# Optimization experiments

Hardware: AMD Instinct MI355X
Metric: run time of the kernel (lower is better)

## Reference

```python
import jax, jax.numpy as jnp
import numpy as np

BN_EPS = 1e-5


def _conv2d(x, w, pad):
    # x: [B,C,H,W], w: [O,I,kh,kw]
    return jax.lax.conv_general_dilated(
        x, w, window_strides=(1, 1), padding=((pad, pad), (pad, pad)),
        dimension_numbers=("NCHW", "OIHW", "NCHW"))


def _feat(x, conv_w, bn_gamma, bn_beta, bn_mean, bn_var, desc_w, desc_b):
    # BasicConv(64->32, k=3, pad=1): conv (no bias) -> BN (inference) -> ReLU
    y = _conv2d(x, conv_w, pad=1)
    inv = bn_gamma / jnp.sqrt(bn_var + BN_EPS)
    y = y * inv[None, :, None, None] + (bn_beta - bn_mean * inv)[None, :, None, None]
    y = jnp.maximum(y, 0.0)
    # desc: 1x1 conv 32->32 with bias
    y = _conv2d(y, desc_w, pad=0) + desc_b[None, :, None, None]
    return y  # [B,32,H,W]


def setup_inputs() -> dict:
    key = jax.random.key(0)
    ks = jax.random.split(key, 4)
    B, Cin, H, W = 8, 64, 160, 576
    left = jax.random.normal(ks[0], (B, Cin, H, W), dtype=jnp.float32)
    right = jax.random.normal(ks[1], (B, Cin, H, W), dtype=jnp.float32)
    conv_w = jax.random.normal(ks[2], (32, 64, 3, 3), dtype=jnp.float32) * 0.05
    bn_gamma = jnp.ones((32,), jnp.float32)
    bn_beta = jnp.zeros((32,), jnp.float32)
    bn_mean = jnp.zeros((32,), jnp.float32)
    bn_var = jnp.ones((32,), jnp.float32)
    desc_w = jax.random.normal(ks[3], (32, 32, 1, 1), dtype=jnp.float32) * 0.1
    desc_b = jnp.zeros((32,), jnp.float32)
    return {"left": left, "right": right, "conv_w": conv_w,
            "bn_gamma": bn_gamma, "bn_beta": bn_beta,
            "bn_mean": bn_mean, "bn_var": bn_var,
            "desc_w": desc_w, "desc_b": desc_b, "maxdisp": 48}


def reference(left, right, conv_w, bn_gamma, bn_beta, bn_mean, bn_var,
              desc_w, desc_b, maxdisp):
    L = _feat(left, conv_w, bn_gamma, bn_beta, bn_mean, bn_var, desc_w, desc_b)
    R = _feat(right, conv_w, bn_gamma, bn_beta, bn_mean, bn_var, desc_w, desc_b)
    # reduce_mean is a frozen 1x1 conv with weight 1/32 == mean over channels.
    cv = [jnp.mean(L * R, axis=1)]  # d = 0, [B,H,W]
    for d in range(1, maxdisp):  # maxdisp is a static Python int (structural)
        c = jnp.mean(L[:, :, :, d:] * R[:, :, :, :-d], axis=1)  # [B,H,W-d]
        cv.append(jnp.pad(c, ((0, 0), (0, 0), (d, 0))))  # zero-pad left edge
    return jnp.stack(cv, axis=1)  # [B, maxdisp, H, W]
```

## Files before the change

### kernel.cpp

```cpp
#include <hip/hip_runtime.h>
#include <stdint.h>

#define HH   160
#define WW   576
#define CIN  64
#define BATCH 8
#define MAXD 48

typedef unsigned int  uint;
typedef unsigned short ushort;
typedef __attribute__((ext_vector_type(8))) short bf16x8;
typedef __attribute__((ext_vector_type(4))) float f32x4;
typedef __attribute__((ext_vector_type(16))) float f32x16;

static constexpr size_t WTB_OFF  = 0;
static constexpr size_t DWT_OFF  = 36864;
static constexpr size_t B1_OFF   = 38912;
static constexpr size_t B2_OFF   = 39040;
static constexpr size_t FEAT_OFF = 40960;
static constexpr size_t FEAT_ELEMS = (size_t)BATCH * HH * WW * 32;

__device__ __forceinline__ uint f2bf(float f) {
    uint u = __float_as_uint(f);
    u = (u + 0x7fffu + ((u >> 16) & 1u)) >> 16;
    return u;
}
__device__ __forceinline__ float bf2f_lo(uint u) { return __uint_as_float(u << 16); }
__device__ __forceinline__ float bf2f_hi(uint u) { return __uint_as_float(u & 0xffff0000u); }
__device__ __forceinline__ uint pk2(float a, float b) { return f2bf(a) | (f2bf(b) << 16); }

__global__ void prep_kernel(const float* __restrict__ conv_w,
                            const float* __restrict__ gamma,
                            const float* __restrict__ beta,
                            const float* __restrict__ mean,
                            const float* __restrict__ var,
                            const float* __restrict__ desc_w,
                            const float* __restrict__ desc_b,
                            char* __restrict__ ws) {
    int tid = blockIdx.x * 256 + threadIdx.x;
    ushort* wtB = (ushort*)(ws + WTB_OFF);
    ushort* dwt = (ushort*)(ws + DWT_OFF);
    float*  b1  = (float*)(ws + B1_OFF);
    float*  b2  = (float*)(ws + B2_OFF);
    if (tid < 36 * 64 * 8) {
        int j    = tid & 7;
        int l    = (tid >> 3) & 63;
        int f    = tid >> 9;
        int s    = f & 3;
        int tap  = f >> 2;
        int ch = l & 31;
        int ci = s * 16 + (l >> 5) * 8 + j;
        float inv = gamma[ch] * rsqrtf(var[ch] + 1e-5f);
        wtB[tid] = (ushort)f2bf(conv_w[(size_t)(ch * 64 + ci) * 9 + tap] * inv);
    }
    if (tid < 1024) {
        int j = tid & 7;
        int l = (tid >> 3) & 63;
        int s = tid >> 9;
        int o = l & 31;
        int mid = (j & 3) + 8 * (j >> 2) + 16 * s + 4 * (l >> 5);
        dwt[tid] = (ushort)f2bf(desc_w[o * 32 + mid]);
    }
    if (tid < 32) {
        float inv = gamma[tid] * rsqrtf(var[tid] + 1e-5f);
        b1[tid] = beta[tid] - mean[tid] * inv;
        b2[tid] = desc_b[tid];
    }
}

#define NXB 6
#define NYB 40
#define NWG (NXB * NYB * 2 * BATCH)
__global__ __launch_bounds__(256, 4)
void feat_mfma(const float* __restrict__ left,
               const float* __restrict__ right,
               const char* __restrict__ ws,
               ushort* __restrict__ featL,
               ushort* __restrict__ featR) {
    __shared__ __align__(16) ushort tile[2 * 600 * 8];

    int bid = blockIdx.x;
    int nid = (bid & 7) * (NWG / 8) + (bid >> 3);
    int x    = nid % NXB;
    int rest = nid / NXB;
    int hy   = rest % NYB;
    int z    = rest / NYB;
    int b    = z & 7;
    const float* __restrict__ in = (z < 8 ? left : right) + (size_t)b * CIN * HH * WW;
    ushort* __restrict__ feat = (z < 8 ? featL : featR);
    const int w0 = x * 96;
    const int h0 = hy * 4;
    const int PL = HH * WW;

    const int lane = threadIdx.x & 63;
    const int wv   = threadIdx.x >> 6;
    const int n    = lane & 31;
    const int hi   = lane >> 5;

    const ushort* __restrict__ wtB = (const ushort*)(ws + WTB_OFF);

    f32x16 acc[3] = {};

    for (int chunk = 0; chunk < 4; ++chunk) {
        for (int t = threadIdx.x; t < 1536; t += 256) {
            int lpx  = t & 63;
            int seg  = t >> 6;
            int part = seg & 1;
            int oct  = (seg >> 1) & 1;
            int r    = seg >> 2;
            int px   = part * 64 + lpx;
            if (px < 100) {
                int gh = h0 + r - 1;
                int gw = w0 - 1 + px;
                float f0 = 0.f, f1 = 0.f, f2 = 0.f, f3 = 0.f,
                      f4 = 0.f, f5 = 0.f, f6 = 0.f, f7 = 0.f;
                if (((unsigned)gh < HH) && ((unsigned)gw < WW)) {
                    const float* src = in + (size_t)(chunk * 16 + oct * 8) * PL
                                          + (size_t)gh * WW + gw;
                    f0 = src[0];
                    f1 = src[(size_t)PL];
                    f2 = src[(size_t)2 * PL];
                    f3 = src[(size_t)3 * PL];
                    f4 = src[(size_t)4 * PL];
                    f5 = src[(size_t)5 * PL];
                    f6 = src[(size_t)6 * PL];
                    f7 = src[(size_t)7 * PL];
                }
                uint4 o4;
                o4.x = pk2(f0, f1);
                o4.y = pk2(f2, f3);
                o4.z = pk2(f4, f5);
                o4.w = pk2(f6, f7);
                *(uint4*)&tile[(size_t)(oct * 600 + r * 100 + px) * 8] = o4;
            }
        }
        __syncthreads();

#pragma unroll
        for (int tap = 0; tap < 9; ++tap) {
            const int r = tap / 3, kw = tap % 3;
            bf16x8 a = *(const bf16x8*)(wtB + (size_t)((tap * 4 + chunk) * 64 + lane) * 8);
#pragma unroll
            for (int tl = 0; tl < 3; ++tl) {
                int px = (wv + r) * 100 + tl * 32 + n + kw;
                bf16x8 bb = *(const bf16x8*)&tile[(size_t)(hi * 600 + px) * 8];
                acc[tl] = __builtin_amdgcn_mfma_f32_32x32x16_bf16(a, bb, acc[tl], 0, 0, 0);
            }
        }
        __syncthreads();
    }

    const float* __restrict__ b1 = (const float*)(ws + B1_OFF);
    const float* __restrict__ b2 = (const float*)(ws + B2_OFF);
    f32x4 b1q[4], b2q[4];
#pragma unroll
    for (int q = 0; q < 4; ++q) {
        b1q[q] = *(const f32x4*)(b1 + 8 * q + 4 * hi);
        b2q[q] = *(const f32x4*)(b2 + 8 * q + 4 * hi);
    }
    const ushort* __restrict__ dwt = (const ushort*)(ws + DWT_OFF);
    bf16x8 da0 = *(const bf16x8*)(dwt + (size_t)lane * 8);
    bf16x8 da1 = *(const bf16x8*)(dwt + (size_t)(64 + lane) * 8);

#pragma unroll
    for (int tl = 0; tl < 3; ++tl) {
        bf16x8 p0, p1;
#pragma unroll
        for (int j = 0; j < 8; ++j) {
            float v0 = fmaxf(acc[tl][j]     + b1q[j >> 2][j & 3],       0.f);
            float v1 = fmaxf(acc[tl][8 + j] + b1q[2 + (j >> 2)][j & 3], 0.f);
            p0[j] = (short)f2bf(v0);
            p1[j] = (short)f2bf(v1);
        }
        f32x16 acc2;
#pragma unroll
        for (int j = 0; j < 16; ++j) acc2[j] = b2q[j >> 2][j & 3];
        acc2 = __builtin_amdgcn_mfma_f32_32x32x16_bf16(da0, p0, acc2, 0, 0, 0);
        acc2 = __builtin_amdgcn_mfma_f32_32x32x16_bf16(da1, p1, acc2, 0, 0, 0);

        size_t pix = ((size_t)b * HH + h0 + wv) * WW + w0 + tl * 32 + n;
        ushort* fp = feat + pix * 32 + 4 * hi;
#pragma unroll
        for (int q = 0; q < 4; ++q) {
            uint u0 = pk2(acc2[4 * q],     acc2[4 * q + 1]);
            uint u1 = pk2(acc2[4 * q + 2], acc2[4 * q + 3]);
            *(uint2*)(fp + 8 * q) = make_uint2(u0, u1);
        }
    }
}

#define CVT 192
__global__ __launch_bounds__(CVT)
void cv_kernel(const ushort* __restrict__ featL,
               const ushort* __restrict__ featR,
               float* __restrict__ out) {
    __shared__ ushort r_lds[WW * 40];

    const int t  = threadIdx.x;
    const int bh = blockIdx.x;
    const int b  = bh / HH;
    const int h  = bh - b * HH;
    const ushort* __restrict__ Lrow = featL + ((size_t)b * HH + h) * WW * 32;
    const ushort* __restrict__ Rrow = featR + ((size_t)b * HH + h) * WW * 32;

#pragma unroll
    for (int k = 0; k < 3; ++k) {
        int w = t + k * CVT;
        const uint4* src = (const uint4*)(Rrow + (size_t)w * 32);
        uint4* dst = (uint4*)(r_lds + (size_t)w * 40);
#pragma unroll
        for (int j = 0; j < 4; ++j) dst[j] = src[j];
    }

    float Lf[3][32];
#pragma unroll
    for (int k = 0; k < 3; ++k) {
        int w = t + k * CVT;
        const uint4* src = (const uint4*)(Lrow + (size_t)w * 32);
#pragma unroll
        for (int j = 0; j < 4; ++j) {
            uint4 v = src[j];
            uint vv[4] = {v.x, v.y, v.z, v.w};
#pragma unroll
            for (int q = 0; q < 4; ++q) {
                Lf[k][j * 8 + q * 2]     = bf2f_lo(vv[q]);
                Lf[k][j * 8 + q * 2 + 1] = bf2f_hi(vv[q]);
            }
        }
    }
    __syncthreads();

    float* __restrict__ outBase = out + ((size_t)b * MAXD * HH + h) * WW;
    for (int d = 0; d < MAXD; ++d) {
#pragma unroll
        for (int k = 0; k < 3; ++k) {
            int w = t + k * CVT;
            float res = 0.f;
            if (w >= d) {
                const uint4* rp = (const uint4*)(r_lds + (size_t)(w - d) * 40);
                float s0 = 0.f, s1 = 0.f;
#pragma unroll
                for (int j = 0; j < 4; ++j) {
                    uint4 v = rp[j];
                    uint vv[4] = {v.x, v.y, v.z, v.w};
#pragma unroll
                    for (int q = 0; q < 4; ++q) {
                        int idx = j * 8 + q * 2;
                        s0 = fmaf(Lf[k][idx],     bf2f_lo(vv[q]), s0);
                        s1 = fmaf(Lf[k][idx + 1], bf2f_hi(vv[q]), s1);
                    }
                }
                res = (s0 + s1) * (1.f / 32.f);
            }
            outBase[(size_t)d * HH * WW + w] = res;
        }
    }
}

extern "C" void kernel_launch(void* const* d_in, const int* in_sizes, int n_in,
                              void* d_out, int out_size, void* d_ws, size_t ws_size,
                              hipStream_t stream) {
    const float* left   = (const float*)d_in[0];
    const float* right  = (const float*)d_in[1];
    const float* conv_w = (const float*)d_in[2];
    const float* gamma  = (const float*)d_in[3];
    const float* beta   = (const float*)d_in[4];
    const float* mean   = (const float*)d_in[5];
    const float* var    = (const float*)d_in[6];
    const float* desc_w = (const float*)d_in[7];
    const float* desc_b = (const float*)d_in[8];
    float*  out   = (float*)d_out;
    char*   ws    = (char*)d_ws;
    ushort* featL = (ushort*)(ws + FEAT_OFF);
    ushort* featR = featL + FEAT_ELEMS;

    prep_kernel<<<72, 256, 0, stream>>>(conv_w, gamma, beta, mean, var, desc_w, desc_b, ws);
    feat_mfma<<<NWG, 256, 0, stream>>>(left, right, ws, featL, featR);
    cv_kernel<<<BATCH * HH, CVT, 0, stream>>>(featL, featR, out);
}
```

Baseline: 252.2 us.

## Double-buffer LDS input tile and overlap global loads with MFMA taps

```diff
diff --git a/kernel.cpp b/kernel.cpp
--- a/kernel.cpp
+++ b/kernel.cpp
@@ -77,7 +77,7 @@
                const char* __restrict__ ws,
                ushort* __restrict__ featL,
                ushort* __restrict__ featR) {
-    __shared__ __align__(16) ushort tile[2 * 600 * 8];
+    __shared__ __align__(16) ushort tile[2][9600];
 
     int bid = blockIdx.x;
     int nid = (bid & 7) * (NWG / 8) + (bid >> 3);
@@ -92,63 +92,84 @@
     const int h0 = hy * 4;
     const int PL = HH * WW;
 
-    const int lane = threadIdx.x & 63;
-    const int wv   = threadIdx.x >> 6;
+    const int tid  = threadIdx.x;
+    const int lane = tid & 63;
+    const int wv   = tid >> 6;
     const int n    = lane & 31;
     const int hi   = lane >> 5;
 
+    const int part = (tid >> 6) & 1;
+    const int octg = tid >> 7;
+    const int spx  = part * 64 + lane;
+    const bool pxok = (spx < 100);
+    const int gw   = w0 - 1 + spx;
+    const bool gwok = ((unsigned)gw < WW);
+
     const ushort* __restrict__ wtB = (const ushort*)(ws + WTB_OFF);
 
     f32x16 acc[3] = {};
-
-    for (int chunk = 0; chunk < 4; ++chunk) {
-        for (int t = threadIdx.x; t < 1536; t += 256) {
-            int lpx  = t & 63;
-            int seg  = t >> 6;
-            int part = seg & 1;
-            int oct  = (seg >> 1) & 1;
-            int r    = seg >> 2;
-            int px   = part * 64 + lpx;
-            if (px < 100) {
-                int gh = h0 + r - 1;
-                int gw = w0 - 1 + px;
-                float f0 = 0.f, f1 = 0.f, f2 = 0.f, f3 = 0.f,
-                      f4 = 0.f, f5 = 0.f, f6 = 0.f, f7 = 0.f;
-                if (((unsigned)gh < HH) && ((unsigned)gw < WW)) {
-                    const float* src = in + (size_t)(chunk * 16 + oct * 8) * PL
-                                          + (size_t)gh * WW + gw;
-                    f0 = src[0];
-                    f1 = src[(size_t)PL];
-                    f2 = src[(size_t)2 * PL];
-                    f3 = src[(size_t)3 * PL];
-                    f4 = src[(size_t)4 * PL];
-                    f5 = src[(size_t)5 * PL];
-                    f6 = src[(size_t)6 * PL];
-                    f7 = src[(size_t)7 * PL];
-                }
+    float rf[3][8];
+
+    auto LOADH = [&](int chunk, int half) {
+#pragma unroll
+        for (int it = 0; it < 3; ++it) {
+            int r  = half * 3 + it;
+            int gh = h0 + r - 1;
+            bool ok = pxok && gwok && ((unsigned)gh < HH);
+            const float* src = in + (size_t)(chunk * 16 + octg * 8) * PL
+                                  + (size_t)gh * WW + gw;
+#pragma unroll
+            for (int j = 0; j < 8; ++j)
+                rf[it][j] = ok ? src[(size_t)j * PL] : 0.f;
+        }
+    };
+    auto WRITEH = [&](int buf, int half) {
+#pragma unroll
+        for (int it = 0; it < 3; ++it) {
+            if (pxok) {
+                int r = half * 3 + it;
                 uint4 o4;
-                o4.x = pk2(f0, f1);
-                o4.y = pk2(f2, f3);
-                o4.z = pk2(f4, f5);
-                o4.w = pk2(f6, f7);
-                *(uint4*)&tile[(size_t)(oct * 600 + r * 100 + px) * 8] = o4;
+                o4.x = pk2(rf[it][0], rf[it][1]);
+                o4.y = pk2(rf[it][2], rf[it][3]);
+                o4.z = pk2(rf[it][4], rf[it][5]);
+                o4.w = pk2(rf[it][6], rf[it][7]);
+                *(uint4*)&tile[buf][(size_t)(octg * 600 + r * 100 + spx) * 8] = o4;
             }
         }
-        __syncthreads();
-
-#pragma unroll
-        for (int tap = 0; tap < 9; ++tap) {
+    };
+    auto MF = [&](int buf, int chunk, int ta, int tb) {
+#pragma unroll
+        for (int tap = ta; tap < tb; ++tap) {
             const int r = tap / 3, kw = tap % 3;
             bf16x8 a = *(const bf16x8*)(wtB + (size_t)((tap * 4 + chunk) * 64 + lane) * 8);
 #pragma unroll
             for (int tl = 0; tl < 3; ++tl) {
                 int px = (wv + r) * 100 + tl * 32 + n + kw;
-                bf16x8 bb = *(const bf16x8*)&tile[(size_t)(hi * 600 + px) * 8];
+                bf16x8 bb = *(const bf16x8*)&tile[buf][(size_t)(hi * 600 + px) * 8];
                 acc[tl] = __builtin_amdgcn_mfma_f32_32x32x16_bf16(a, bb, acc[tl], 0, 0, 0);
             }
         }
+    };
+
+    LOADH(0, 0); WRITEH(0, 0);
+    LOADH(0, 1); WRITEH(0, 1);
+    __syncthreads();
+
+    for (int c = 0; c < 3; ++c) {
+        const int cur = c & 1, nxt = cur ^ 1;
+        LOADH(c + 1, 0);
+        __builtin_amdgcn_sched_barrier(0);
+        MF(cur, c, 0, 4);
+        __builtin_amdgcn_sched_barrier(0);
+        WRITEH(nxt, 0);
+        LOADH(c + 1, 1);
+        __builtin_amdgcn_sched_barrier(0);
+        MF(cur, c, 4, 9);
+        __builtin_amdgcn_sched_barrier(0);
+        WRITEH(nxt, 1);
         __syncthreads();
     }
+    MF(1, 3, 0, 9);
 
     const float* __restrict__ b1 = (const float*)(ws + B1_OFF);
     const float* __restrict__ b2 = (const float*)(ws + B2_OFF);
```

Result: no change. 249.9 us (-0.9%).
